# Performance work log

Measured on AMD Instinct MI355X. Metric: run time of the kernel, lower is better.

## Reference

```python
import jax, jax.numpy as jnp
import numpy as np

B, D, RES, NS, MAXS, ITERS = 64, 512, 16, 8, 64, 3
N = RES * RES            # ntokens
HID = max(D, 128)        # mlp hidden = max(dim, hidden_dim)
EPS = 1e-8
BETA = 0.99
SCALE = D ** -0.5


def _grid(res):
    rs = [np.linspace(0.0, 1.0, num=r) for r in (res, res)]
    g = np.stack(np.meshgrid(*rs, sparse=False, indexing='ij'), axis=-1)
    g = g.reshape(res, res, 2)[None].astype(np.float32)
    return jnp.asarray(np.concatenate([g, 1.0 - g], axis=-1))  # (1,res,res,4)


def _ln(x, g, b, axes):
    m = jnp.mean(x, axes, keepdims=True)
    v = jnp.var(x, axes, keepdims=True)
    return (x - m) * jax.lax.rsqrt(v + 1e-5) * g + b


def _gru(x, h, wih, whh, bih, bhh):
    gi = x @ wih.T + bih
    gh = h @ whh.T + bhh
    ir, iz, inn = jnp.split(gi, 3, -1)
    hr, hz, hn = jnp.split(gh, 3, -1)
    r = jax.nn.sigmoid(ir + hr)
    z = jax.nn.sigmoid(iz + hz)
    n = jnp.tanh(inn + r * hn)
    return (1.0 - z) * n + z * h


def setup_inputs() -> dict:
    key = jax.random.key(0)
    ks = iter(jax.random.split(key, 40))
    W = lambda *s: jax.random.normal(next(ks), s, jnp.float32) * 0.02
    Z = lambda *s: jnp.zeros(s, jnp.float32)
    O = lambda *s: jnp.ones(s, jnp.float32)
    inp = dict(
        x=jax.random.normal(next(ks), (B, D, RES, RES), jnp.float32),
        enc_pos_w=W(4, D), enc_pos_b=Z(D),
        enc_norm_g=O(N, D), enc_norm_b=Z(N, D),
        enc_mlp_w1=W(D, D), enc_mlp_b1=Z(D), enc_mlp_w2=W(D, D), enc_mlp_b2=Z(D),
        anch_w1=W(N, N), anch_b1=Z(N), anch_w2=W(N, N), anch_b2=Z(N),
        wq=W(D, D), bq=Z(D), wk=W(D, D), bk=Z(D), wv=W(D, D), bv=Z(D),
        gru_wih=W(3 * D, D), gru_whh=W(3 * D, D), gru_bih=Z(3 * D), gru_bhh=Z(3 * D),
        mlp_w1=W(D, HID), mlp_b1=Z(HID), mlp_w2=W(HID, D), mlp_b2=Z(D),
        ni_g=O(D), ni_b=Z(D), ns_g=O(D), ns_b=Z(D), npf_g=O(D), npf_b=Z(D),
        emb=jax.random.uniform(next(ks), (MAXS, D), jnp.float32, -1.0 / MAXS, 1.0 / MAXS),
        dec_pos_w=W(4, D), dec_pos_b=Z(D),
    )
    return inp


def reference(x, enc_pos_w, enc_pos_b, enc_norm_g, enc_norm_b,
              enc_mlp_w1, enc_mlp_b1, enc_mlp_w2, enc_mlp_b2,
              anch_w1, anch_b1, anch_w2, anch_b2,
              wq, bq, wk, bk, wv, bv,
              gru_wih, gru_whh, gru_bih, gru_bhh,
              mlp_w1, mlp_b1, mlp_w2, mlp_b2,
              ni_g, ni_b, ns_g, ns_b, npf_g, npf_b,
              emb, dec_pos_w, dec_pos_b):
    sg = jax.lax.stop_gradient
    grid = _grid(RES)
    f = jnp.transpose(x, (0, 2, 3, 1))                       # (B,RES,RES,D)
    # encoder_transformation(position=False): flatten + LayerNorm([N,D]) over last 2 dims
    f_np = _ln(f.reshape(B, N, D), enc_norm_g, enc_norm_b, (-2, -1))
    k_nopos = f_np @ wk + bk
    # encoder_transformation(position=True): +pos, LN([N,D]), feature MLP, then norm_input
    pos = grid @ enc_pos_w + enc_pos_b
    fp = _ln((f + pos).reshape(B, N, D), enc_norm_g, enc_norm_b, (-2, -1))
    fp = jax.nn.relu(fp @ enc_mlp_w1 + enc_mlp_b1) @ enc_mlp_w2 + enc_mlp_b2
    fp = _ln(fp, ni_g, ni_b, -1)
    k = fp @ wk + bk
    v = fp @ wv + bv
    # passthrough_eigen_basis on detached k_nopos: normalize, covariance, eigh
    xn = k_nopos / jnp.clip(jnp.linalg.norm(k_nopos, axis=-1, keepdims=True), 1e-12)
    cov = sg(jnp.einsum('bkf,bgf->bkg', xn, xn))             # (B,N,N)
    _, evec = jnp.linalg.eigh(cov)                           # ascending, like symeig
    eig_vec = jnp.transpose(evec[:, :, 1:NS + 1], (0, 2, 1))  # (B,NS,N)
    eig_vec = jax.nn.relu(eig_vec @ anch_w1 + anch_b1) @ anch_w2 + anch_b2
    z = jnp.einsum('bnf,bkn->bkf', f_np, eig_vec)            # masked_projection -> (B,NS,D)
    # sample_slotemb_traditional (euclidean, non-unique, update=0)
    zf = z.reshape(-1, D)
    tslots = emb @ wq + bq                                   # (MAXS,D)
    d2 = (zf ** 2).sum(1, keepdims=True) + (tslots ** 2).sum(1) - 2.0 * zf @ tslots.T
    sampled_dist = d2.min(1)
    idx = jnp.argmin(d2, 1)                                  # (B*NS,)
    # faithful reproduction of the original's index reordering (incl. its cross-batch quirk)
    order = jnp.argsort(sampled_dist.reshape(B, NS), axis=1).reshape(-1)
    idx = idx[order]
    z_q = emb[idx].reshape(B, NS, D)
    t_zq = tslots[idx].reshape(B, NS, D)
    qloss = ((sg(t_zq) - z) ** 2).sum() / B + BETA * ((t_zq - sg(z)) ** 2).sum() / B
    slots = z + sg(z_q - z)                                  # straight-through
    # slot attention iterations
    for _ in range(ITERS):
        slots_prev = slots
        q = _ln(slots, ns_g, ns_b, -1) @ wq + bq
        dots = jnp.einsum('bid,bjd->bij', q, k) * SCALE      # (B,NS,N)
        attn = jax.nn.softmax(dots, axis=1) + EPS            # competition over slots
        attn = attn / attn.sum(-1, keepdims=True)
        updates = jnp.einsum('bjd,bij->bid', v, attn)
        slots = _gru(updates.reshape(-1, D), slots_prev.reshape(-1, D),
                     gru_wih, gru_whh, gru_bih, gru_bhh).reshape(B, NS, D)
        h = _ln(slots, npf_g, npf_b, -1)
        slots = slots + (jax.nn.relu(h @ mlp_w1 + mlp_b1) @ mlp_w2 + mlp_b2)
    # decoder_transformation: broadcast slots over decoder grid + position embed
    dpos = grid @ dec_pos_w + dec_pos_b                      # (1,RES,RES,D)
    df = jnp.broadcast_to(slots.reshape(B * NS, 1, 1, D), (B * NS, RES, RES, D)) + dpos
    feats = jnp.transpose(df, (0, 3, 1, 2))                  # (B*NS,D,RES,RES)
    return feats, slots, idx.reshape(B, NS), qloss
```

## Files before the change

kernel.cpp:

```cpp
#include <hip/hip_runtime.h>
#include <math.h>
#include <stdint.h>


#define NB 64
#define ND 512
#define NN_ 256
#define NSL 8
#define LPB 24

static __device__ __forceinline__ double fsign(double a, double b) {
  return (b >= 0.0) ? fabs(a) : -fabs(a);
}
static __device__ __forceinline__ double dlapy2d(double x, double y) {
  double ax = fabs(x), ay = fabs(y);
  double w = ax > ay ? ax : ay, z = ax > ay ? ay : ax;
  if (z == 0.0) return w;
  double q = z / w;
  return w * sqrt(1.0 + q * q);
}
#define EPS_D 1.1102230246251565e-16

static __device__ void dlartgd(double f, double g, double& cs, double& sn, double& r) {
  if (g == 0.0) { cs = 1.0; sn = 0.0; r = f; }
// ... 206 lines not shown
  for (int i = t; i < 131072; i += 256) {
    float v = xb[i];
    if (addpos) v += posT[i];
    s += v; ss += (double)v * v;
  }
  r1[t] = s; r2[t] = ss; __syncthreads();
  for (int o = 128; o > 0; o >>= 1) { if (t < o) { r1[t] += r1[t + o]; r2[t] += r2[t + o]; } __syncthreads(); }
  if (t == 0) {
    double m = r1[0] / 131072.0;
    double var = r2[0] / 131072.0 - m * m;
    mean_o[b] = (float)m;
    rstd_o[b] = 1.0f / sqrtf((float)var + 1e-5f);
  }
}

__global__ __launch_bounds__(256) void tln_kernel(const float* __restrict__ x,
                                                  const float* __restrict__ posT,
                                                  const float* __restrict__ g,
                                                  const float* __restrict__ be,
                                                  const float* m1, const float* r1,
                                                  const float* m2, const float* r2,
                                                  float* __restrict__ fnp,
                                                  float* __restrict__ fpln) {
  int b = blockIdx.x, dt = blockIdx.y, nt = blockIdx.z;
  __shared__ float t1[32][33], t2[32][33];
  int t = threadIdx.x;
  const float* xb = x + (size_t)b * 131072;
  for (int l = 0; l < 4; ++l) {
    int idx = t + l * 256;
    int row = idx >> 5, col = idx & 31;
    int dd = dt * 32 + row, nn = nt * 32 + col;
    float v = xb[(size_t)dd * 256 + nn];
    t1[row][col] = v;
    t2[row][col] = v + posT[(size_t)dd * 256 + nn];
  }
  __syncthreads();
  float mm1 = m1[b], rr1 = r1[b], mm2 = m2[b], rr2 = r2[b];
  for (int l = 0; l < 4; ++l) {
    int idx = t + l * 256;
    int row = idx >> 5, col = idx & 31;
    int nn = nt * 32 + row, dd = dt * 32 + col;
    float gg = g[(size_t)nn * 512 + dd], bb = be[(size_t)nn * 512 + dd];
    size_t o = (size_t)b * 131072 + (size_t)nn * 512 + dd;
    fnp[o] = (t1[col][row] - mm1) * rr1 * gg + bb;
    fpln[o] = (t2[col][row] - mm2) * rr2 * gg + bb;
  }
}

__global__ __launch_bounds__(256) void gemm_f32(const float* __restrict__ A,
                                                const float* __restrict__ Bm,
                                                const float* __restrict__ bias,
                                                const float* __restrict__ base,
                                                float* __restrict__ C, int M, int Nc, int Kd,
                                                int bt, int act, int addb) {
  __shared__ float As[16][65];
  __shared__ float Bs[16][65];
  int bm = blockIdx.x * 64, bn = blockIdx.y * 64;
  int t = threadIdx.x;
  int tx = t & 15, ty = t >> 4;
  float acc[4][4] = {};
  for (int k0 = 0; k0 < Kd; k0 += 16) {
    for (int l = 0; l < 4; ++l) {
      int idx = t + l * 256;
      { int r = idx >> 4, kk = idx & 15;
        float v = 0.f;
        if (bm + r < M && k0 + kk < Kd) v = A[(size_t)(bm + r) * Kd + k0 + kk];
        As[kk][r] = v; }
      if (bt == 0) {
        int kk = idx >> 6, nn = idx & 63;
        float v = 0.f;
        if (k0 + kk < Kd && bn + nn < Nc) v = Bm[(size_t)(k0 + kk) * Nc + bn + nn];
        Bs[kk][nn] = v;
      } else {
        int nn = idx >> 4, kk = idx & 15;
        float v = 0.f;
        if (bn + nn < Nc && k0 + kk < Kd) v = Bm[(size_t)(bn + nn) * Kd + k0 + kk];
        Bs[kk][nn] = v;
      }
    }
    __syncthreads();
#pragma unroll
    for (int kk = 0; kk < 16; ++kk) {
      float a0[4], b0[4];
#pragma unroll
      for (int q = 0; q < 4; ++q) a0[q] = As[kk][ty * 4 + q];
#pragma unroll
      for (int q = 0; q < 4; ++q) b0[q] = Bs[kk][tx * 4 + q];
#pragma unroll
      for (int q = 0; q < 4; ++q)
#pragma unroll
        for (int p = 0; p < 4; ++p) acc[q][p] += a0[q] * b0[p];
    }
    __syncthreads();
  }
  for (int q = 0; q < 4; ++q) {
    int r = bm + ty * 4 + q;
    if (r >= M) continue;
    for (int p = 0; p < 4; ++p) {
      int c = bn + tx * 4 + p;
      if (c >= Nc) continue;
      float v = acc[q][p];
      if (bias) v += bias[c];
      if (act == 1) v = fmaxf(v, 0.f);
      if (addb) v += base[(size_t)r * Nc + c];
      C[(size_t)r * Nc + c] = v;
    }
  }
}

__global__ __launch_bounds__(256) void gemm_f32_big(const float* __restrict__ A,
                                                    const float* __restrict__ Bm,
                                                    const float* __restrict__ bias,
                                                    const float* __restrict__ base,
                                                    float* __restrict__ C, int M, int Nc, int Kd,
                                                    int bt, int act, int addb) {
  __shared__ float As[16][128];
  __shared__ float Bs[16][128];
  int bm = blockIdx.x * 128, bn = blockIdx.y * 128;
  int t = threadIdx.x;
  int tx = t & 15, ty = t >> 4;
  int lrow = t >> 1, lseg = (t & 1) * 8;
  float acc[8][8] = {};
  for (int k0 = 0; k0 < Kd; k0 += 16) {
    {
      const float* src = A + (size_t)(bm + lrow) * Kd + k0 + lseg;
      float4 p0 = *(const float4*)src;
      float4 p1 = *(const float4*)(src + 4);
      As[lseg + 0][lrow] = p0.x; As[lseg + 1][lrow] = p0.y;
      As[lseg + 2][lrow] = p0.z; As[lseg + 3][lrow] = p0.w;
      As[lseg + 4][lrow] = p1.x; As[lseg + 5][lrow] = p1.y;
      As[lseg + 6][lrow] = p1.z; As[lseg + 7][lrow] = p1.w;
    }
    if (bt == 0) {
      int bk = t >> 4, bcol = (t & 15) * 8;
      const float* src = Bm + (size_t)(k0 + bk) * Nc + bn + bcol;
      float4 p0 = *(const float4*)src;
      float4 p1 = *(const float4*)(src + 4);
      *(float4*)&Bs[bk][bcol] = p0;
      *(float4*)&Bs[bk][bcol + 4] = p1;
    } else {
      const float* src = Bm + (size_t)(bn + lrow) * Kd + k0 + lseg;
      float4 p0 = *(const float4*)src;
      float4 p1 = *(const float4*)(src + 4);
      Bs[lseg + 0][lrow] = p0.x; Bs[lseg + 1][lrow] = p0.y;
      Bs[lseg + 2][lrow] = p0.z; Bs[lseg + 3][lrow] = p0.w;
      Bs[lseg + 4][lrow] = p1.x; Bs[lseg + 5][lrow] = p1.y;
      Bs[lseg + 6][lrow] = p1.z; Bs[lseg + 7][lrow] = p1.w;
    }
    __syncthreads();
#pragma unroll
    for (int kk = 0; kk < 16; ++kk) {
      float a0[8], b0[8];
#pragma unroll
      for (int q = 0; q < 8; ++q) a0[q] = As[kk][ty * 8 + q];
#pragma unroll
      for (int p = 0; p < 8; ++p) b0[p] = Bs[kk][tx * 8 + p];
#pragma unroll
      for (int q = 0; q < 8; ++q)
#pragma unroll
        for (int p = 0; p < 8; ++p) acc[q][p] += a0[q] * b0[p];
    }
    __syncthreads();
  }
  for (int q = 0; q < 8; ++q) {
    int r = bm + ty * 8 + q;
    float* Cr = C + (size_t)r * Nc + bn + tx * 8;
    const float* baser = base + (size_t)r * Nc + bn + tx * 8;
#pragma unroll
    for (int p = 0; p < 8; ++p) {
      float vv = acc[q][p];
      if (bias) vv += bias[bn + tx * 8 + p];
      if (act == 1) vv = fmaxf(vv, 0.f);
      if (addb) vv += baser[p];
      Cr[p] = vv;
    }
  }
}

__global__ __launch_bounds__(256) void rowln_kernel(const float* __restrict__ in,
                                                    const float* __restrict__ g,
                                                    const float* __restrict__ be,
                                                    float* __restrict__ out) {
  int r = blockIdx.x, t = threadIdx.x;
  __shared__ double s1[256], s2[256];
  const float* row = in + (size_t)r * 512;
  float v0 = row[t], v1 = row[t + 256];
  s1[t] = (double)v0 + (double)v1;
  s2[t] = (double)v0 * v0 + (double)v1 * v1;
  __syncthreads();
  for (int o = 128; o > 0; o >>= 1) { if (t < o) { s1[t] += s1[t + o]; s2[t] += s2[t + o]; } __syncthreads(); }
  double m = s1[0] / 512.0, var = s2[0] / 512.0 - m * m;
  float rstd = 1.0f / sqrtf((float)var + 1e-5f);
  float mf = (float)m;
  out[(size_t)r * 512 + t] = (v0 - mf) * rstd * g[t] + be[t];
  out[(size_t)r * 512 + t + 256] = (v1 - mf) * rstd * g[t + 256] + be[t + 256];
}

__global__ __launch_bounds__(256) void xnorm_kernel(float* kno) {
  int r = blockIdx.x, t = threadIdx.x;
  __shared__ double s1[256];
  float* row = kno + (size_t)r * 512;
  float v0 = row[t], v1 = row[t + 256];
  s1[t] = (double)v0 * v0 + (double)v1 * v1;
  __syncthreads();
  for (int o = 128; o > 0; o >>= 1) { if (t < o) s1[t] += s1[t + o]; __syncthreads(); }
  float nrm = fmaxf((float)sqrt(s1[0]), 1e-12f);
  row[t] = v0 / nrm; row[t + 256] = v1 / nrm;
}

__global__ __launch_bounds__(256) void cov_kernel(const float* __restrict__ xn, double* __restrict__ cov) {
  int b = blockIdx.x, it = blockIdx.y, jt = blockIdx.z;
  __shared__ float Xi[64][65], Xj[64][65];
  int t = threadIdx.x;
  int tx = t & 15, ty = t >> 4;
  double acc[4][4] = {};
  const float* xb = xn + (size_t)b * 131072;
  for (int f0 = 0; f0 < 512; f0 += 64) {
    for (int l = 0; l < 16; ++l) {
      int idx = t + l * 256;
      int r = idx >> 6, ff = idx & 63;
      Xi[r][ff] = xb[(size_t)(it * 64 + r) * 512 + f0 + ff];
      Xj[r][ff] = xb[(size_t)(jt * 64 + r) * 512 + f0 + ff];
    }
    __syncthreads();
    for (int ff = 0; ff < 64; ++ff) {
      double a0[4], b0[4];
#pragma unroll
      for (int q = 0; q < 4; ++q) { a0[q] = (double)Xi[ty * 4 + q][ff]; b0[q] = (double)Xj[tx * 4 + q][ff]; }
#pragma unroll
      for (int q = 0; q < 4; ++q)
#pragma unroll
        for (int p = 0; p < 4; ++p) acc[q][p] += a0[q] * b0[p];
    }
    __syncthreads();
  }
  double* cb = cov + (size_t)b * 65536;
  for (int q = 0; q < 4; ++q)
    for (int p = 0; p < 4; ++p)
      cb[(size_t)(it * 64 + ty * 4 + q) * 256 + jt * 64 + tx * 4 + p] = acc[q][p];
}

__global__ __launch_bounds__(1024) void dsytrd_kernel(double* Aall, double* dE, double* eE,
                                                      double* tauE) {
  int b = blockIdx.x, t = threadIdx.x;
  int lane = t & 63, wid = t >> 6;
  double* A = Aall + (size_t)b * 65536;
  __shared__ double buf0[256], buf1[256], buf2[256], buf3[256];
  __shared__ double v2[256];
  __shared__ double redw[16];
  const int n = 256;
  double* v = buf0; double* w = buf1;
  double* vp = buf2; double* wp = buf3;
  int pend = 0;
  for (int i = 0; i < n - 1; ++i) {
    for (int r = i + t; r < n; r += 1024) {
      double a = A[(size_t)r * 256 + i];
      if (pend) {
        a = a - (vp[r] * wp[i] + wp[r] * vp[i]);
        A[(size_t)r * 256 + i] = a;
      }
      v2[r] = a;
    }
    __syncthreads();
    double s = 0.0;
    for (int r = i + 2 + t; r < n; r += 1024) { double xv = v2[r]; s += xv * xv; }
    for (int o = 1; o < 64; o <<= 1) s += __shfl_xor(s, o);
    if (lane == 0) redw[wid] = s;
    __syncthreads();
    double xns = 0.0;
    for (int k = 0; k < 16; ++k) xns += redw[k];
    double alpha = v2[i + 1];
    double tau, beta, scl;
    if (xns == 0.0) { tau = 0.0; beta = alpha; scl = 0.0; }
    else {
      double xnorm = sqrt(xns);
      double rr = dlapy2d(alpha, xnorm);
      beta = (alpha >= 0.0) ? -rr : rr;
      tau = (beta - alpha) / beta;
      scl = 1.0 / (alpha - beta);
    }
    if (tau != 0.0) {
      for (int r = i + 1 + t; r < n; r += 1024) {
        double vr = (r == i + 1) ? 1.0 : v2[r] * scl;
        v[r] = vr;
        if (r >= i + 2) A[(size_t)r * 256 + i] = vr;
      }
      __syncthreads();
      for (int r = i + 1 + wid; r < n; r += 16) {
        double* Ar = A + (size_t)r * 256;
        double acc = 0.0;
        if (pend) {
          double vpr = vp[r], wpr = wp[r];
          for (int c = i + 1 + lane; c < n; c += 64) {
            double a = Ar[c] - (vpr * wp[c] + wpr * vp[c]);
            Ar[c] = a;
            acc += a * v[c];
          }
        } else {
          for (int c = i + 1 + lane; c < n; c += 64) acc += Ar[c] * v[c];
        }
        for (int o = 1; o < 64; o <<= 1) acc += __shfl_xor(acc, o);
        if (lane == 0) w[r] = tau * acc;
      }
      __syncthreads();
      double sd = 0.0;
      for (int r = i + 1 + t; r < n; r += 1024) sd += w[r] * v[r];
      for (int o = 1; o < 64; o <<= 1) sd += __shfl_xor(sd, o);
      if (lane == 0) redw[wid] = sd;
      __syncthreads();
      double dot = 0.0;
      for (int k = 0; k < 16; ++k) dot += redw[k];
      double alpha2 = -0.5 * tau * dot;
      for (int r = i + 1 + t; r < n; r += 1024) w[r] += alpha2 * v[r];
    } else if (pend) {
      for (int r = i + 1 + wid; r < n; r += 16) {
        double* Ar = A + (size_t)r * 256;
        double vpr = vp[r], wpr = wp[r];
        for (int c = i + 1 + lane; c < n; c += 64)
          Ar[c] = Ar[c] - (vpr * wp[c] + wpr * vp[c]);
      }
    }
    if (t == 0) { eE[b * 256 + i] = beta; tauE[b * 256 + i] = tau; }
    __syncthreads();
    if (tau != 0.0) {
      double* tv = v; v = vp; vp = tv;
      double* tw = w; w = wp; wp = tw;
      pend = 1;
    } else {
      pend = 0;
    }
  }
  for (int r = t; r < n; r += 1024) {
    double dd = A[(size_t)r * 256 + r];
    if (pend && r == n - 1) dd = dd - (vp[r] * wp[r] + wp[r] * vp[r]);
    dE[b * 256 + r] = dd;
  }
}

__global__ __launch_bounds__(64) void tear_kernel(double* dE, const double* eE) {
  int b = threadIdx.x;
  if (b >= 64) return;
  for (int m = 1; m < 16; ++m) {
    int p = m * 16 - 1;
    double ae = fabs(eE[b * 256 + p]);
    dE[b * 256 + p] -= ae;
    dE[b * 256 + p + 1] -= ae;
  }
}

__global__ __launch_bounds__(64) void leaf_kernel(double* dE, double* eE, double* Qe, int* indxq) {
  __shared__ double Zs[LPB * 256];
  __shared__ double des[LPB * 33];
  int t = threadIdx.x;
  int g = blockIdx.x * LPB + t;
  if (t >= LPB || g >= 1024) return;
  int b = g >> 4, lf = g & 15, off = lf * 16;
  double* zz = Zs + t * 256;
  double* dd = des + t * 33;
  double* ee = dd + 16;
  int sw = t & 15;
  for (int i = 1; i <= 16; ++i) dd[i] = dE[b * 256 + off + i - 1];
  for (int i = 1; i <= 15; ++i) ee[i] = eE[b * 256 + off + i - 1];
  ee[16] = 0.0;
  dsteqr16_lds(dd, ee, zz, sw);
  for (int i = 1; i <= 16; ++i) dE[b * 256 + off + i - 1] = dd[i];
  double* Qb = Qe + (size_t)b * 65536;
  for (int r = 0; r < 16; ++r)
    for (int c = 0; c < 16; ++c) Qb[(size_t)(off + r) * 256 + off + c] = zz[((r << 4) + c) ^ sw];
  for (int i = 0; i < 16; ++i) indxq[b * 256 + off + i] = i + 1;
}

__global__ __launch_bounds__(256) void merge_scan_kernel(int nm, int nmerge, double* Qsrc, double* dE,
                                                         const double* eE, int* indxq,
                                                         double* dlamda_g, double* w_g, double* rho_g,
                                                         int* surv_g, int* defl_g, int* Kb) {
  int b = blockIdx.x, mg = blockIdx.y;
  int off = mg * nm, n1 = nm / 2, n2 = nm - n1;
  double* Q = Qsrc + (size_t)b * 65536;
  double* dg = dE + b * 256 + off;
  int* iqg = indxq + b * 256 + off;
  int t = threadIdx.x;

  __shared__ double dl[257], zl[257], dlamA[257], wl2[257];
  __shared__ int iq[257], indxc[257], indxl[257], indxpl[257];
  __shared__ double rotc[256], rots[256];
  __shared__ int rotp[256], rotn[256];
  __shared__ int sh_nrot, sh_K, sh_zero;

  for (int ii = 1 + t; ii <= nm; ii += 256) { dl[ii] = dg[ii - 1]; iq[ii] = iqg[ii - 1]; }
  __syncthreads();

  if (t == 0) {
    double rho = eE[b * 256 + off + n1 - 1];
    for (int j = 1; j <= n1; ++j) zl[j] = Q[(size_t)(off + n1 - 1) * 256 + off + j - 1];
    for (int j = 1; j <= n2; ++j) zl[n1 + j] = Q[(size_t)(off + n1) * 256 + off + n1 + j - 1];
    if (rho < 0.0)
      for (int j = n1 + 1; j <= nm; ++j) zl[j] = -zl[j];
    double tconst = 1.0 / sqrt(2.0);
    for (int j = 1; j <= nm; ++j) zl[j] *= tconst;
    rho = fabs(2.0 * rho);
    rho_g[b * nmerge + mg] = rho;
    for (int i = n1 + 1; i <= nm; ++i) iq[i] += n1;
    for (int i = 1; i <= nm; ++i) dlamA[i] = dl[iq[i]];
    dlamrg_dev(n1, n2, dlamA, 1, 1, indxc);
    for (int i = 1; i <= nm; ++i) indxl[i] = iq[indxc[i]];
    int imax = 1, jmax = 1;
    for (int i = 2; i <= nm; ++i) {
      if (fabs(zl[i]) > fabs(zl[imax])) imax = i;
      if (fabs(dl[i]) > fabs(dl[jmax])) jmax = i;
    }
    double tol = 8.0 * EPS_D * fmax(fabs(dl[jmax]), fabs(zl[imax]));
    if (rho * fabs(zl[imax]) <= tol) {
      sh_K = 0; sh_zero = 1; sh_nrot = 0;
    } else {
      sh_zero = 0;
      int nrot = 0;
      int K = 0, K2 = nm + 1, pj = 0, j = 1;
      bool havepj = false;
      for (j = 1; j <= nm; ++j) {
        int nj = indxl[j];
        if (rho * fabs(zl[nj]) <= tol) {
          K2--; indxpl[K2] = nj;
          if (j == nm) break;
        } else { pj = nj; havepj = true; break; }
      }
      if (havepj) {
        for (;;) {
          j = j + 1;
          if (j > nm) break;
          int nj = indxl[j];
          if (rho * fabs(zl[nj]) <= tol) { K2--; indxpl[K2] = nj; }
          else {
            double s_ = zl[pj], c_ = zl[nj];
            double tau_ = dlapy2d(c_, s_);
            double t_ = dl[nj] - dl[pj];
            c_ = c_ / tau_; s_ = -s_ / tau_;
            if (fabs(t_ * c_ * s_) <= tol) {
              zl[nj] = tau_; zl[pj] = 0.0;
              rotp[nrot] = pj; rotn[nrot] = nj; rotc[nrot] = c_; rots[nrot] = s_; ++nrot;
              double t2 = dl[pj] * c_ * c_ + dl[nj] * s_ * s_;
              dl[nj] = dl[pj] * s_ * s_ + dl[nj] * c_ * c_;
              dl[pj] = t2;
              K2--;
              int i_ = 1;
              for (;;) {
                if (K2 + i_ <= nm) {
                  if (dl[pj] < dl[indxpl[K2 + i_]]) {
                    indxpl[K2 + i_ - 1] = indxpl[K2 + i_];
                    indxpl[K2 + i_] = pj;
                    i_++;
                  } else { indxpl[K2 + i_ - 1] = pj; break; }
                } else { indxpl[K2 + i_ - 1] = pj; break; }
              }
              pj = nj;
            } else {
              K++; dlamA[K] = dl[pj]; wl2[K] = zl[pj]; indxpl[K] = pj; pj = nj;
            }
          }
        }
        K++; dlamA[K] = dl[pj]; wl2[K] = zl[pj]; indxpl[K] = pj;
      }
      sh_K = K; sh_nrot = nrot;
    }
  }
  __syncthreads();
  int nrot = sh_nrot, K = sh_K;
  for (int r = t; r < nm; r += 256) {
    size_t rowb = (size_t)(off + r) * 256;
    for (int k = 0; k < nrot; ++k) {
      int cp = off + rotp[k] - 1, cn = off + rotn[k] - 1;
      double c_ = rotc[k], s_ = rots[k];
      double x = Q[rowb + cp], y = Q[rowb + cn];
      Q[rowb + cp] = c_ * x + s_ * y;
      Q[rowb + cn] = c_ * y - s_ * x;
    }
  }
  if (sh_zero) {
    if (t == 0) Kb[b * nmerge + mg] = 0;
    for (int j = 1 + t; j <= nm; j += 256) {
      int il = indxl[j];
      defl_g[b * 256 + off + j - 1] = il;
      dg[j - 1] = dl[il];
      iqg[j - 1] = j;
    }
  } else {
    if (t == 0) Kb[b * nmerge + mg] = K;
    for (int i = 1 + t; i <= K; i += 256) {
// ... 347 lines not shown
__global__ __launch_bounds__(64) void asum_kernel(const float* attn, float* asum) {
  int bi = blockIdx.x, lane = threadIdx.x;
  float s = 0.f;
  for (int j = lane; j < 256; j += 64) s += attn[(size_t)bi * 256 + j] + 1e-8f;
  for (int off = 32; off > 0; off >>= 1) s += __shfl_down(s, off);
  if (lane == 0) asum[bi] = s;
}

__global__ __launch_bounds__(256) void updates_kernel(const float* attn, const float* asum,
                                                      const float* v, float* upd) {
  int b = blockIdx.x;
  __shared__ float at[8][257];
  int t = threadIdx.x;
  for (int i = t; i < 8 * 256; i += 256) {
    int ii = i / 256, j = i % 256;
    at[ii][j] = (attn[((size_t)b * 8 + ii) * 256 + j] + 1e-8f) / asum[b * 8 + ii];
  }
  __syncthreads();
  for (int d = t; d < 512; d += 256) {
    float acc[8] = {0, 0, 0, 0, 0, 0, 0, 0};
    for (int j = 0; j < 256; ++j) {
      float vv = v[((size_t)b * 256 + j) * 512 + d];
#pragma unroll
      for (int ii = 0; ii < 8; ++ii) acc[ii] += at[ii][j] * vv;
    }
    for (int ii = 0; ii < 8; ++ii) upd[((size_t)b * 8 + ii) * 512 + d] = acc[ii];
  }
}

__global__ __launch_bounds__(256) void gru_kernel(const float* gi, const float* gh, const float* h,
                                                  float* out) {
  int i = blockIdx.x * 256 + threadIdx.x;
  if (i >= 512 * 512) return;
  int t = i / 512, d = i % 512;
  const float* gir = gi + (size_t)t * 1536;
  const float* ghr = gh + (size_t)t * 1536;
  float r = 1.f / (1.f + expf(-(gir[d] + ghr[d])));
  float zg = 1.f / (1.f + expf(-(gir[512 + d] + ghr[512 + d])));
  float n = tanhf(gir[1024 + d] + r * ghr[1024 + d]);
  out[i] = (1.f - zg) * n + zg * h[i];
}

__global__ __launch_bounds__(64) void feats_kernel(const float* slots, const float* dposT,
                                                   float* out) {
  int blk = blockIdx.x;
  int bs = blk >> 9, d = blk & 511;
  float s = slots[(size_t)bs * 512 + d];
  const float* dp = dposT + (size_t)d * 256;
  int n0 = threadIdx.x * 4;
  float4 o;
  o.x = s + dp[n0]; o.y = s + dp[n0 + 1]; o.z = s + dp[n0 + 2]; o.w = s + dp[n0 + 3];
  *(float4*)(out + (size_t)blk * 256 + n0) = o;
}


extern "C" void kernel_launch(void* const* d_in, const int* in_sizes, int n_in, void* d_out,
                              int out_size, void* d_ws, size_t ws_size, hipStream_t stream) {
  const float* x = (const float*)d_in[0];
  const float* enc_pos_w = (const float*)d_in[1];
  const float* enc_pos_b = (const float*)d_in[2];
  const float* enc_norm_g = (const float*)d_in[3];
  const float* enc_norm_b = (const float*)d_in[4];
  const float* enc_mlp_w1 = (const float*)d_in[5];
  const float* enc_mlp_b1 = (const float*)d_in[6];
  const float* enc_mlp_w2 = (const float*)d_in[7];
  const float* enc_mlp_b2 = (const float*)d_in[8];
  const float* anch_w1 = (const float*)d_in[9];
  const float* anch_b1 = (const float*)d_in[10];
  const float* anch_w2 = (const float*)d_in[11];
  const float* anch_b2 = (const float*)d_in[12];
  const float* wq = (const float*)d_in[13];
  const float* bq = (const float*)d_in[14];
  const float* wk = (const float*)d_in[15];
  const float* bk = (const float*)d_in[16];
  const float* wv = (const float*)d_in[17];
  const float* bv = (const float*)d_in[18];
  const float* gru_wih = (const float*)d_in[19];
  const float* gru_whh = (const float*)d_in[20];
  const float* gru_bih = (const float*)d_in[21];
  const float* gru_bhh = (const float*)d_in[22];
  const float* mlp_w1 = (const float*)d_in[23];
  const float* mlp_b1 = (const float*)d_in[24];
  const float* mlp_w2 = (const float*)d_in[25];
  const float* mlp_b2 = (const float*)d_in[26];
  const float* ni_g = (const float*)d_in[27];
  const float* ni_b = (const float*)d_in[28];
  const float* ns_g = (const float*)d_in[29];
  const float* ns_b = (const float*)d_in[30];
  const float* npf_g = (const float*)d_in[31];
  const float* npf_b = (const float*)d_in[32];
  const float* emb = (const float*)d_in[33];
  const float* dec_pos_w = (const float*)d_in[34];
  const float* dec_pos_b = (const float*)d_in[35];

  float* out = (float*)d_out;
  const size_t FEATS = (size_t)512 * 512 * 256;
  float* out_slots = out + FEATS;
  float* out_idx = out + FEATS + 262144;
  float* out_qloss = out + FEATS + 262144 + 512;

  char* ws = (char*)d_ws;
  size_t off = 0;
  auto alloc = [&](size_t bytes) { size_t o = off; off = (off + bytes + 255) & ~(size_t)255; return (void*)(ws + o); };
  const size_t S = (size_t)64 * 256 * 512 * 4;
  float* fnp = (float*)alloc(S);
  float* R2 = (float*)alloc(S);
  float* R3 = (float*)alloc(S);
  float* R4 = (float*)alloc(S);
  float* R5 = (float*)alloc(S);
  float* kbuf = (float*)alloc(S);
  float* vbuf = (float*)alloc(S);
  float* posT = (float*)alloc(512 * 256 * 4);
  float* dposT = (float*)alloc(512 * 256 * 4);
  float* m1 = (float*)alloc(64 * 4);
  float* r1 = (float*)alloc(64 * 4);
  float* m2 = (float*)alloc(64 * 4);
  float* r2 = (float*)alloc(64 * 4);
  double* dE = (double*)alloc(64 * 256 * 8);
  double* eE = (double*)alloc(64 * 256 * 8);
  double* tauE = (double*)alloc(64 * 256 * 8);
  double* dlamda_g = (double*)alloc(64 * 256 * 8);
  double* w_g = (double*)alloc(64 * 256 * 8);
  double* zhat_g = (double*)alloc(64 * 256 * 8);
  double* tau_g = (double*)alloc(64 * 256 * 8);
  double* rho_g = (double*)alloc(64 * 8 * 8);
  int* indxq = (int*)alloc(64 * 256 * 4);
  int* surv_g = (int*)alloc(64 * 256 * 4);
  int* defl_g = (int*)alloc(64 * 256 * 4);
  int* orig_g = (int*)alloc(64 * 256 * 4);
  int* Kb = (int*)alloc(64 * 8 * 4);
  int* fidx = (int*)alloc(512 * 4);
  float* E = (float*)alloc(64 * 8 * 256 * 4);
  float* Eh = (float*)alloc(64 * 8 * 256 * 4);
  float* E2 = (float*)alloc(64 * 8 * 256 * 4);
  float* z = (float*)alloc(512 * 512 * 4);
  float* tslots = (float*)alloc(64 * 512 * 4);
  double* sdist = (double*)alloc(512 * 8);
  int* idxr = (int*)alloc(512 * 4);
  float* sA = (float*)alloc(512 * 512 * 4);
  float* sB = (float*)alloc(512 * 512 * 4);
  float* lnbuf = (float*)alloc(512 * 512 * 4);
  float* qbuf = (float*)alloc(512 * 512 * 4);
  float* dotsb = (float*)alloc(64 * 8 * 256 * 4);
  float* attnb = (float*)alloc(64 * 8 * 256 * 4);
  float* asumb = (float*)alloc(64 * 8 * 4);
  float* updb = (float*)alloc(512 * 512 * 4);
  float* gib = (float*)alloc((size_t)512 * 1536 * 4);
  float* ghb = (float*)alloc((size_t)512 * 1536 * 4);
  float* hidb = (float*)alloc(512 * 512 * 4);
  (void)ws_size; (void)in_sizes; (void)n_in; (void)out_size;

  auto gemm = [&](const float* A, const float* Bm, const float* bias, const float* base, float* C,
                  int M, int Nc, int Kd, int bt, int act, int addb) {
    if ((M % 128) == 0 && (Nc % 128) == 0 && (Kd % 16) == 0) {
      dim3 g(M / 128, Nc / 128);
      gemm_f32_big<<<g, 256, 0, stream>>>(A, Bm, bias, base, C, M, Nc, Kd, bt, act, addb);
    } else {
      dim3 g((M + 63) / 64, (Nc + 63) / 64);
      gemm_f32<<<g, 256, 0, stream>>>(A, Bm, bias, base, C, M, Nc, Kd, bt, act, addb);
    }
  };

  pos_kernel<<<(131072 + 255) / 256, 256, 0, stream>>>(enc_pos_w, enc_pos_b, posT);
  pos_kernel<<<(131072 + 255) / 256, 256, 0, stream>>>(dec_pos_w, dec_pos_b, dposT);
  stats_kernel<<<64, 256, 0, stream>>>(x, posT, m1, r1, 0);
  stats_kernel<<<64, 256, 0, stream>>>(x, posT, m2, r2, 1);
  tln_kernel<<<dim3(64, 16, 8), 256, 0, stream>>>(x, posT, enc_norm_g, enc_norm_b, m1, r1, m2, r2,
                                                  fnp, R3);
  gemm(fnp, wk, bk, nullptr, R2, 16384, 512, 512, 0, 0, 0);
  gemm(R3, enc_mlp_w1, enc_mlp_b1, nullptr, R4, 16384, 512, 512, 0, 1, 0);
  gemm(R4, enc_mlp_w2, enc_mlp_b2, nullptr, R5, 16384, 512, 512, 0, 0, 0);
  rowln_kernel<<<16384, 256, 0, stream>>>(R5, ni_g, ni_b, R5);
  gemm(R5, wk, bk, nullptr, kbuf, 16384, 512, 512, 0, 0, 0);
  gemm(R5, wv, bv, nullptr, vbuf, 16384, 512, 512, 0, 0, 0);
  xnorm_kernel<<<16384, 256, 0, stream>>>(R2);
  double* covA = (double*)R3;
  cov_kernel<<<dim3(64, 4, 4), 256, 0, stream>>>(R2, covA);
  double* Qe = (double*)R4;
  double* Q2 = (double*)R5;
  double* Cbuf = (double*)R2;
  hipMemsetAsync(Qe, 0, S, stream);
  hipMemsetAsync(Q2, 0, S, stream);
  dsytrd_kernel<<<64, 1024, 0, stream>>>(covA, dE, eE, tauE);
  tear_kernel<<<1, 64, 0, stream>>>(dE, eE);
  leaf_kernel<<<(1024 + LPB - 1) / LPB, LPB, 0, stream>>>(dE, eE, Qe, indxq);
  for (int L = 0; L < 4; ++L) {
    int nm = 32 << L;
    int nmerge = 256 / nm;
    double* src = (L % 2 == 0) ? Qe : Q2;
    double* dst = (L % 2 == 0) ? Q2 : Qe;
    int gScan = (64 * nmerge + 63) / 64;
    merge_scan_kernel<<<dim3(64, nmerge), 256, 0, stream>>>(nm, nmerge, src, dE, eE, indxq,
                                                            dlamda_g, w_g, rho_g, surv_g, defl_g, Kb);
    secular_kernel<<<64, 256, 0, stream>>>(nm, nmerge, dlamda_g, w_g, rho_g, Kb, dE, tau_g, orig_g);
    zhat_kernel<<<64, 256, 0, stream>>>(nm, nmerge, dlamda_g, w_g, tau_g, orig_g, Kb, zhat_g);
    coeff_kernel<<<64, 256, 0, stream>>>(nm, nmerge, dlamda_g, zhat_g, tau_g, orig_g, Kb, Cbuf);
    int tcnt = nm / 32;
    merge_gemm_kernel<<<dim3(64, nmerge, tcnt * tcnt), 256, 0, stream>>>(nm, nmerge, src, Cbuf,
                                                                         surv_g, Kb, dst);
    defl_copy_kernel<<<dim3(64, nmerge), 256, 0, stream>>>(nm, nmerge, src, defl_g, Kb, dst);
    dlamrg_kernel<<<gScan, 64, 0, stream>>>(nm, nmerge, dE, Kb, indxq);
  }
  dormtr_kernel<<<64, 256, 0, stream>>>(covA, tauE, Qe, indxq, E);
  gemm(E, anch_w1, anch_b1, nullptr, Eh, 512, 256, 256, 0, 1, 0);
  gemm(Eh, anch_w2, anch_b2, nullptr, E2, 512, 256, 256, 0, 0, 0);
  zproj_kernel<<<64, 256, 0, stream>>>(fnp, E2, z);
  gemm(emb, wq, bq, nullptr, tslots, 64, 512, 512, 0, 0, 0);
  d2_kernel<<<512, 64, 0, stream>>>(z, tslots, sdist, idxr);
  order_kernel<<<1, 64, 0, stream>>>(sdist, idxr, fidx, out_idx);
  slots0_kernel<<<1024, 256, 0, stream>>>(z, emb, fidx, sA);
  qloss_kernel<<<1, 256, 0, stream>>>(z, tslots, fidx, out_qloss);
  for (int it = 0; it < 3; ++it) {
    rowln_kernel<<<512, 256, 0, stream>>>(sA, ns_g, ns_b, lnbuf);
    gemm(lnbuf, wq, bq, nullptr, qbuf, 512, 512, 512, 0, 0, 0);
    dots_kernel<<<dim3(64, 4), 256, 0, stream>>>(qbuf, kbuf, dotsb);
    softmax_kernel<<<64, 256, 0, stream>>>(dotsb, attnb);
    asum_kernel<<<512, 64, 0, stream>>>(attnb, asumb);
    updates_kernel<<<64, 256, 0, stream>>>(attnb, asumb, vbuf, updb);
    gemm(updb, gru_wih, gru_bih, nullptr, gib, 512, 1536, 512, 1, 0, 0);
    gemm(sA, gru_whh, gru_bhh, nullptr, ghb, 512, 1536, 512, 1, 0, 0);
    gru_kernel<<<1024, 256, 0, stream>>>(gib, ghb, sA, sB);
    rowln_kernel<<<512, 256, 0, stream>>>(sB, npf_g, npf_b, lnbuf);
    gemm(lnbuf, mlp_w1, mlp_b1, nullptr, hidb, 512, 512, 512, 0, 1, 0);
    gemm(hidb, mlp_w2, mlp_b2, sB, sA, 512, 512, 512, 0, 0, 1);
  }
  feats_kernel<<<262144, 64, 0, stream>>>(sA, dposT, out);
  hipMemcpyAsync(out_slots, sA, 262144 * 4, hipMemcpyDeviceToDevice, stream);
}
```

Before: 14.24 ms.

## Defer tridiagonal rank-2 updates two steps; interleave GEMM thread tiles; gate big GEMM

The Householder tridiagonalization kernel now keeps up to two pending rank-2 updates. It applies both in one combined sweep that reads and writes the trailing matrix, rather than writing it back after every step, which roughly halves global read-modify-write traffic on the matrix. The 128x128 SGEMM now gives each thread two 4-wide strips 64 apart instead of one contiguous 8-wide strip, to reduce LDS bank conflicts on the fragment loads; the epilogue writes become strided. The big-tile GEMM path is now used only when the grid has at least 128 blocks, so small GEMMs fall back to the 64-tile kernel for better occupancy across CUs.

New measurement: 14.08 ms. About the same (-1.1%).

```diff
diff --git a/kernel.cpp b/kernel.cpp
--- a/kernel.cpp
+++ b/kernel.cpp
@@ -382,9 +382,9 @@
     for (int kk = 0; kk < 16; ++kk) {
       float a0[8], b0[8];
 #pragma unroll
-      for (int q = 0; q < 8; ++q) a0[q] = As[kk][ty * 8 + q];
-#pragma unroll
-      for (int p = 0; p < 8; ++p) b0[p] = Bs[kk][tx * 8 + p];
+      for (int q = 0; q < 4; ++q) { a0[q] = As[kk][ty * 4 + q]; a0[4 + q] = As[kk][64 + ty * 4 + q]; }
+#pragma unroll
+      for (int p = 0; p < 4; ++p) { b0[p] = Bs[kk][tx * 4 + p]; b0[4 + p] = Bs[kk][64 + tx * 4 + p]; }
 #pragma unroll
       for (int q = 0; q < 8; ++q)
 #pragma unroll
@@ -393,16 +393,15 @@
     __syncthreads();
   }
   for (int q = 0; q < 8; ++q) {
-    int r = bm + ty * 8 + q;
-    float* Cr = C + (size_t)r * Nc + bn + tx * 8;
-    const float* baser = base + (size_t)r * Nc + bn + tx * 8;
+    int r = bm + ((q < 4) ? (ty * 4 + q) : (64 + ty * 4 + (q - 4)));
 #pragma unroll
     for (int p = 0; p < 8; ++p) {
+      int c = bn + ((p < 4) ? (tx * 4 + p) : (64 + tx * 4 + (p - 4)));
       float vv = acc[q][p];
-      if (bias) vv += bias[bn + tx * 8 + p];
+      if (bias) vv += bias[c];
       if (act == 1) vv = fmaxf(vv, 0.f);
-      if (addb) vv += baser[p];
-      Cr[p] = vv;
+      if (addb) vv += base[(size_t)r * Nc + c];
+      C[(size_t)r * Nc + c] = vv;
     }
   }
 }
@@ -475,18 +474,20 @@
   int b = blockIdx.x, t = threadIdx.x;
   int lane = t & 63, wid = t >> 6;
   double* A = Aall + (size_t)b * 65536;
-  __shared__ double buf0[256], buf1[256], buf2[256], buf3[256];
+  __shared__ double bufA[256], bufB[256], bufC[256], bufD[256], bufE[256], bufF[256];
   __shared__ double v2[256];
   __shared__ double redw[16];
   const int n = 256;
-  double* v = buf0; double* w = buf1;
-  double* vp = buf2; double* wp = buf3;
-  int pend = 0;
+  double* v = bufA;   double* w = bufB;
+  double* vp1 = bufC; double* wp1 = bufD;
+  double* vp2 = bufE; double* wp2 = bufF;
+  int cnt = 0;
   for (int i = 0; i < n - 1; ++i) {
     for (int r = i + t; r < n; r += 1024) {
       double a = A[(size_t)r * 256 + i];
-      if (pend) {
-        a = a - (vp[r] * wp[i] + wp[r] * vp[i]);
+      if (cnt >= 1) {
+        a = a - (vp1[r] * wp1[i] + wp1[r] * vp1[i]);
+        if (cnt == 2) a = a - (vp2[r] * wp2[i] + wp2[r] * vp2[i]);
         A[(size_t)r * 256 + i] = a;
       }
       v2[r] = a;
@@ -510,6 +511,7 @@
       scl = 1.0 / (alpha - beta);
     }
     if (tau != 0.0) {
+      int dow = (cnt == 2);
       for (int r = i + 1 + t; r < n; r += 1024) {
         double vr = (r == i + 1) ? 1.0 : v2[r] * scl;
         v[r] = vr;
@@ -519,11 +521,18 @@
       for (int r = i + 1 + wid; r < n; r += 16) {
         double* Ar = A + (size_t)r * 256;
         double acc = 0.0;
-        if (pend) {
-          double vpr = vp[r], wpr = wp[r];
+        if (cnt == 2) {
+          double v1r = vp1[r], w1r = wp1[r], v2r = vp2[r], w2r = wp2[r];
           for (int c = i + 1 + lane; c < n; c += 64) {
-            double a = Ar[c] - (vpr * wp[c] + wpr * vp[c]);
+            double a = Ar[c] - (v1r * wp1[c] + w1r * vp1[c]);
+            a = a - (v2r * wp2[c] + w2r * vp2[c]);
             Ar[c] = a;
+            acc += a * v[c];
+          }
+        } else if (cnt == 1) {
+          double v1r = vp1[r], w1r = wp1[r];
+          for (int c = i + 1 + lane; c < n; c += 64) {
+            double a = Ar[c] - (v1r * wp1[c] + w1r * vp1[c]);
             acc += a * v[c];
           }
         } else {
@@ -542,27 +551,45 @@
       for (int k = 0; k < 16; ++k) dot += redw[k];
       double alpha2 = -0.5 * tau * dot;
       for (int r = i + 1 + t; r < n; r += 1024) w[r] += alpha2 * v[r];
-    } else if (pend) {
-      for (int r = i + 1 + wid; r < n; r += 16) {
-        double* Ar = A + (size_t)r * 256;
-        double vpr = vp[r], wpr = wp[r];
-        for (int c = i + 1 + lane; c < n; c += 64)
-          Ar[c] = Ar[c] - (vpr * wp[c] + wpr * vp[c]);
+      if (t == 0) { eE[b * 256 + i] = beta; tauE[b * 256 + i] = tau; }
+      __syncthreads();
+      if (dow) {
+        double* tv = v; v = vp1; vp1 = tv;
+        double* tw = w; w = wp1; wp1 = tw;
+        cnt = 1;
+      } else if (cnt == 0) {
+        double* tv = v; v = vp1; vp1 = tv;
+        double* tw = w; w = wp1; wp1 = tw;
+        cnt = 1;
+      } else {
+        double* tv = v; v = vp2; vp2 = tv;
+        double* tw = w; w = wp2; wp2 = tw;
+        cnt = 2;
       }
-    }
-    if (t == 0) { eE[b * 256 + i] = beta; tauE[b * 256 + i] = tau; }
-    __syncthreads();
-    if (tau != 0.0) {
-      double* tv = v; v = vp; vp = tv;
-      double* tw = w; w = wp; wp = tw;
-      pend = 1;
     } else {
-      pend = 0;
+      if (cnt >= 1) {
+        for (int r = i + 1 + wid; r < n; r += 16) {
+          double* Ar = A + (size_t)r * 256;
+          double v1r = vp1[r], w1r = wp1[r];
+          double v2r = (cnt == 2) ? vp2[r] : 0.0, w2r = (cnt == 2) ? wp2[r] : 0.0;
+          for (int c = i + 1 + lane; c < n; c += 64) {
+            double a = Ar[c] - (v1r * wp1[c] + w1r * vp1[c]);
+            if (cnt == 2) a = a - (v2r * wp2[c] + w2r * vp2[c]);
+            Ar[c] = a;
+          }
+        }
+      }
+      if (t == 0) { eE[b * 256 + i] = beta; tauE[b * 256 + i] = tau; }
+      __syncthreads();
+      cnt = 0;
     }
   }
   for (int r = t; r < n; r += 1024) {
     double dd = A[(size_t)r * 256 + r];
-    if (pend && r == n - 1) dd = dd - (vp[r] * wp[r] + wp[r] * vp[r]);
+    if (r == n - 1) {
+      if (cnt >= 1) dd = dd - (vp1[r] * wp1[r] + wp1[r] * vp1[r]);
+      if (cnt == 2) dd = dd - (vp2[r] * wp2[r] + wp2[r] * vp2[r]);
+    }
     dE[b * 256 + r] = dd;
   }
 }
@@ -1216,7 +1243,8 @@
 
   auto gemm = [&](const float* A, const float* Bm, const float* bias, const float* base, float* C,
                   int M, int Nc, int Kd, int bt, int act, int addb) {
-    if ((M % 128) == 0 && (Nc % 128) == 0 && (Kd % 16) == 0) {
+    if ((M % 128) == 0 && (Nc % 128) == 0 && (Kd % 16) == 0 &&
+        (M / 128) * (Nc / 128) >= 128) {
       dim3 g(M / 128, Nc / 128);
       gemm_f32_big<<<g, 256, 0, stream>>>(A, Bm, bias, base, C, M, Nc, Kd, bt, act, addb);
     } else {
```
